# Optimization experiments

Hardware: AMD Instinct MI355X
Metric: run time of the kernel (lower is better)

Reference implementation:

```python
import jax, jax.numpy as jnp
import numpy as np

N_USER = 100000
N_ITEM = 100000
E = 500000
EMB, HID, OUT = 128, 128, 64


def _mean_agg(msg_src, src, dst, n_dst):
    """Gather per-edge messages from src nodes, segment-mean onto dst nodes."""
    m = msg_src[src]  # [E, d]
    s = jax.ops.segment_sum(m, dst, num_segments=n_dst)
    cnt = jax.ops.segment_sum(jnp.ones((src.shape[0],), m.dtype), dst,
                              num_segments=n_dst)
    # DGL mean reducer yields 0 for nodes with no in-edges
    return jnp.where(cnt[:, None] > 0, s / jnp.maximum(cnt, 1.0)[:, None], 0.0)


def _layer(feat_u, feat_i, W0, b0, Wui, bui, Wiu, biu,
           src_ui, dst_ui, src_iu, dst_iu):
    # shared self-transform (weight0) -> residual h0 on every ntype
    h0_u = feat_u @ W0 + b0
    h0_i = feat_i @ W0 + b0
    # per-etype transform of source features
    wh_u = feat_u @ Wui + bui  # messages along user->item
    wh_i = feat_i @ Wiu + biu  # messages along item->user
    h_i = _mean_agg(wh_u, src_ui, dst_ui, N_ITEM) + h0_i
    h_u = _mean_agg(wh_i, src_iu, dst_iu, N_USER) + h0_u
    return h_u, h_i


def setup_inputs() -> dict:
    key = jax.random.key(0)
    ks = jax.random.split(key, 12)
    sc_e = 1.0 / np.sqrt(EMB)
    sc_h = 1.0 / np.sqrt(HID)
    return {
        "emb_user": jax.random.normal(ks[0], (N_USER, EMB), jnp.float32),
        "emb_item": jax.random.normal(ks[1], (N_ITEM, EMB), jnp.float32),
        "W1_0": jax.random.normal(ks[2], (EMB, HID), jnp.float32) * sc_e,
        "b1_0": jnp.zeros((HID,), jnp.float32),
        "W1_ui": jax.random.normal(ks[3], (EMB, HID), jnp.float32) * sc_e,
        "b1_ui": jnp.zeros((HID,), jnp.float32),
        "W1_iu": jax.random.normal(ks[4], (EMB, HID), jnp.float32) * sc_e,
        "b1_iu": jnp.zeros((HID,), jnp.float32),
        "W2_0": jax.random.normal(ks[5], (HID, OUT), jnp.float32) * sc_h,
        "b2_0": jnp.zeros((OUT,), jnp.float32),
        "W2_ui": jax.random.normal(ks[6], (HID, OUT), jnp.float32) * sc_h,
        "b2_ui": jnp.zeros((OUT,), jnp.float32),
        "W2_iu": jax.random.normal(ks[7], (HID, OUT), jnp.float32) * sc_h,
        "b2_iu": jnp.zeros((OUT,), jnp.float32),
        "src_ui": jax.random.randint(ks[8], (E,), 0, N_USER, jnp.int32),
        "dst_ui": jax.random.randint(ks[9], (E,), 0, N_ITEM, jnp.int32),
        "src_iu": jax.random.randint(ks[10], (E,), 0, N_ITEM, jnp.int32),
        "dst_iu": jax.random.randint(ks[11], (E,), 0, N_USER, jnp.int32),
    }


def reference(emb_user, emb_item,
              W1_0, b1_0, W1_ui, b1_ui, W1_iu, b1_iu,
              W2_0, b2_0, W2_ui, b2_ui, W2_iu, b2_iu,
              src_ui, dst_ui, src_iu, dst_iu):
    h_u, h_i = _layer(emb_user, emb_item, W1_0, b1_0, W1_ui, b1_ui,
                      W1_iu, b1_iu, src_ui, dst_ui, src_iu, dst_iu)
    h_u = jax.nn.leaky_relu(h_u, 0.01)  # torch F.leaky_relu default slope
    h_i = jax.nn.leaky_relu(h_i, 0.01)
    h_u, h_i = _layer(h_u, h_i, W2_0, b2_0, W2_ui, b2_ui,
                      W2_iu, b2_iu, src_ui, dst_ui, src_iu, dst_iu)
    return h_u, h_i
```

## Files before the change

kernel.cpp:

```cpp
#include <hip/hip_runtime.h>

#define N_USER 100000
#define N_ITEM 100000
#define NEDGE  500000
#define DEGCAP 32

#define B_FILL 256
#define B_CONV 12500
#define B_WT   384
#define B_TOT  (B_FILL + B_CONV + B_WT)

typedef __attribute__((ext_vector_type(8))) short short8;
typedef __attribute__((ext_vector_type(4))) float f32x4;

__device__ __forceinline__ unsigned short f2bf(float f) {
  union { float f; unsigned int u; } x{f};
  unsigned int r = x.u + 0x7fffu + ((x.u >> 16) & 1u);
  return (unsigned short)(r >> 16);
}
__device__ __forceinline__ float bf2f(unsigned short u) {
  union { unsigned int u; float f; } x{(unsigned int)u << 16};
  return x.f;
}

__global__ __launch_bounds__(256) void setup_k(
    const int* __restrict__ src_ui, const int* __restrict__ dst_ui,
    int* __restrict__ cur_i, int* __restrict__ csr_ui,
    const int* __restrict__ src_iu, const int* __restrict__ dst_iu,
    int* __restrict__ cur_u, int* __restrict__ csr_iu,
    const float* __restrict__ emb_u, const float* __restrict__ emb_i,
    unsigned short* __restrict__ ebu, unsigned short* __restrict__ ebi,
    const float* __restrict__ W10, const float* __restrict__ W1ui,
    const float* __restrict__ W1iu, const float* __restrict__ W20,
    const float* __restrict__ W2ui, const float* __restrict__ W2iu,
    unsigned short* __restrict__ WT1i, unsigned short* __restrict__ WT1u,
    unsigned short* __restrict__ WT2i, unsigned short* __restrict__ WT2u) {
  int b = blockIdx.x, tid = threadIdx.x;
  if (b < B_FILL) {
    int chunk = b * 4096;
#pragma unroll 1
    for (int it = 0; it < 4; ++it) {
      int e0 = chunk + it * 1024 + tid;
      int d[4], s[4];
      int* curp[4]; int* csrp[4];
      bool ok[4];
#pragma unroll
      for (int k = 0; k < 4; ++k) {
        int e = e0 + k * 256;
        ok[k] = (e < 2 * NEDGE);
        bool g0 = (e < NEDGE);
        int ee = g0 ? e : e - NEDGE;
        const int* dp = g0 ? dst_ui : dst_iu;
        const int* sp = g0 ? src_ui : src_iu;
        curp[k] = g0 ? cur_i : cur_u;
        csrp[k] = g0 ? csr_ui : csr_iu;
        d[k] = ok[k] ? dp[ee] : 0;
        s[k] = ok[k] ? sp[ee] : 0;
      }
      int p[4];
#pragma unroll
      for (int k = 0; k < 4; ++k)
        p[k] = ok[k] ? atomicAdd(&curp[k][d[k]], 1) : DEGCAP;
#pragma unroll
      for (int k = 0; k < 4; ++k)
        if (ok[k] && p[k] < DEGCAP) csrp[k][d[k] * DEGCAP + p[k]] = s[k];
    }
  } else if (b < B_FILL + B_CONV) {
    int blk = b - B_FILL;
    const float* src; unsigned short* dstp;
    if (blk < 6250) { src = emb_u; dstp = ebu; }
    else { blk -= 6250; src = emb_i; dstp = ebi; }
    size_t g = (size_t)blk * 2048 + (size_t)tid * 8;
    float4 x = *(const float4*)(src + g);
    float4 y = *(const float4*)(src + g + 4);
    short8 v{(short)f2bf(x.x), (short)f2bf(x.y), (short)f2bf(x.z), (short)f2bf(x.w),
             (short)f2bf(y.x), (short)f2bf(y.y), (short)f2bf(y.z), (short)f2bf(y.w)};
    *(short8*)(dstp + g) = v;
  } else {
    int t = (b - B_FILL - B_CONV) * 256 + tid;
    if (t < 32768) {
      int n = t >> 8, k = t & 255;
      float v = (k < 128) ? W10[k * 128 + n] : W1ui[(k - 128) * 128 + n];
      WT1i[t] = f2bf(v);
    } else if (t < 65536) {
      int q = t - 32768; int n = q >> 8, k = q & 255;
      float v = (k < 128) ? W10[k * 128 + n] : W1iu[(k - 128) * 128 + n];
      WT1u[q] = f2bf(v);
    } else if (t < 81920) {
      int q = t - 65536; int n = q >> 8, k = q & 255;
      float v = (k < 128) ? W20[k * 64 + n] : W2ui[(k - 128) * 64 + n];
      WT2i[q] = f2bf(v);
    } else {
      int q = t - 81920; int n = q >> 8, k = q & 255;
      float v = (k < 128) ? W20[k * 64 + n] : W2iu[(k - 128) * 64 + n];
      WT2u[q] = f2bf(v);
    }
  }
}

__global__ __launch_bounds__(256) void aggc_k(
    const unsigned short* __restrict__ featA, const int* __restrict__ curA,
    const int* __restrict__ csrA, unsigned short* __restrict__ outA,
    const unsigned short* __restrict__ featB, const int* __restrict__ curB,
    const int* __restrict__ csrB, unsigned short* __restrict__ outB,
    int nbA) {
  __shared__ int sidx[16][32];
  int b = blockIdx.x;
  const unsigned short* feat; const int* cur; const int* csr; unsigned short* out;
  if (b < nbA) { feat = featA; cur = curA; csr = csrA; out = outA; }
  else { b -= nbA; feat = featB; cur = curB; csr = csrB; out = outB; }
  int grp = threadIdx.x >> 4;
  int ln  = threadIdx.x & 15;
  int node = b * 16 + grp;
  int deg = min(cur[node], DEGCAP);

  int2 sl = *(const int2*)(csr + (size_t)node * DEGCAP + ln * 2);
  sidx[grp][ln * 2] = sl.x;
  sidx[grp][ln * 2 + 1] = sl.y;
  __syncthreads();

  const int* lidx = sidx[grp];
  float a[8] = {0, 0, 0, 0, 0, 0, 0, 0};
  int j = 0;
  if (j + 4 <= deg) {
    int i0 = lidx[0], i1 = lidx[1], i2 = lidx[2], i3 = lidx[3];
    for (;;) {
      bool more = (j + 8 <= deg);
      int n0, n1, n2, n3;
      if (more) { n0 = lidx[j + 4]; n1 = lidx[j + 5]; n2 = lidx[j + 6]; n3 = lidx[j + 7]; }
      short8 v0 = *(const short8*)(feat + (size_t)i0 * 128 + ln * 8);
      short8 v1 = *(const short8*)(feat + (size_t)i1 * 128 + ln * 8);
      short8 v2 = *(const short8*)(feat + (size_t)i2 * 128 + ln * 8);
      short8 v3 = *(const short8*)(feat + (size_t)i3 * 128 + ln * 8);
#pragma unroll
      for (int d = 0; d < 8; ++d)
        a[d] += (bf2f((unsigned short)v0[d]) + bf2f((unsigned short)v1[d])) +
                (bf2f((unsigned short)v2[d]) + bf2f((unsigned short)v3[d]));
      j += 4;
      if (!more) break;
      i0 = n0; i1 = n1; i2 = n2; i3 = n3;
    }
  }
  if (j + 2 <= deg) {
    int i0 = lidx[j], i1 = lidx[j + 1];
    short8 v0 = *(const short8*)(feat + (size_t)i0 * 128 + ln * 8);
    short8 v1 = *(const short8*)(feat + (size_t)i1 * 128 + ln * 8);
#pragma unroll
    for (int d = 0; d < 8; ++d)
      a[d] += bf2f((unsigned short)v0[d]) + bf2f((unsigned short)v1[d]);
    j += 2;
  }
  if (j < deg) {
    short8 v = *(const short8*)(feat + (size_t)lidx[j] * 128 + ln * 8);
#pragma unroll
    for (int d = 0; d < 8; ++d) a[d] += bf2f((unsigned short)v[d]);
  }
  float sc = deg ? 1.f / (float)deg : 0.f;
  short8 pk;
#pragma unroll
  for (int d = 0; d < 8; ++d) pk[d] = (short)f2bf(a[d] * sc);
  *(short8*)(out + (size_t)node * 128 + ln * 8) = pk;
}

template <int N, bool LRELU, bool OUTBF16>
__global__ __launch_bounds__(256) void gemm2_k(
    const unsigned short* __restrict__ A1a, const unsigned short* __restrict__ A2a,
    const unsigned short* __restrict__ WTa, const float* __restrict__ b0a,
    const float* __restrict__ bea, const int* __restrict__ cura,
    void* __restrict__ outa,
    const unsigned short* __restrict__ A1b, const unsigned short* __restrict__ A2b,
    const unsigned short* __restrict__ WTb, const float* __restrict__ b0b,
    const float* __restrict__ beb, const int* __restrict__ curb,
    void* __restrict__ outb, int M, int nbA) {
  constexpr int BM = 64;
  constexpr int CPW = N / 4;
  constexpr int NCF = CPW / 16;
  __shared__ short As[BM * 128];
  __shared__ short Ws[N * 128];
  __shared__ float degmask[BM];

  int blk = blockIdx.x;
  const unsigned short* A1; const unsigned short* A2; const unsigned short* WT;
  const float* b0; const float* be; const int* cur; void* outv;
  if (blk < nbA) { A1 = A1a; A2 = A2a; WT = WTa; b0 = b0a; be = bea; cur = cura; outv = outa; }
  else { blk -= nbA; A1 = A1b; A2 = A2b; WT = WTb; b0 = b0b; be = beb; cur = curb; outv = outb; }

  const int tid = threadIdx.x;
  const int lane = tid & 63;
  const int wave = tid >> 6;
  const int row0 = blk * BM;
  const int colbase = wave * CPW;

  short8 aA[4], aB[4];
#pragma unroll
  for (int it = 0; it < 4; ++it) {
    int chunk = tid + it * 256;
    int row = chunk >> 4, c16 = chunk & 15;
    int gr = row0 + row; if (gr > M - 1) gr = M - 1;
    aA[it] = *(const short8*)(A1 + (size_t)gr * 128 + c16 * 8);
    aB[it] = *(const short8*)(A2 + (size_t)gr * 128 + c16 * 8);
  }

  if (tid < BM) {
    int r = row0 + tid;
    degmask[tid] = (r < M && cur[r] > 0) ? 1.f : 0.f;
  }

  f32x4 acc[4][NCF] = {};

#pragma unroll
  for (int kh = 0; kh < 2; ++kh) {
    __syncthreads();
#pragma unroll
    for (int it = 0; it < 4; ++it) {
      int chunk = tid + it * 256;
      int row = chunk >> 4, c16 = chunk & 15;
      int byteoff = row * 256 + ((c16 * 16) ^ ((row & 7) << 4));
      *(short8*)((char*)As + byteoff) = (kh == 0) ? aA[it] : aB[it];
    }
#pragma unroll
    for (int it = 0; it < (N * 16) / 256; ++it) {
      int chunk = tid + it * 256;
      int n = chunk >> 4, c16 = chunk & 15;
      short8 v = *(const short8*)(WT + (size_t)n * 256 + kh * 128 + c16 * 8);
      int byteoff = n * 256 + ((c16 * 16) ^ ((n & 7) << 4));
      *(short8*)((char*)Ws + byteoff) = v;
    }
    __syncthreads();

#pragma unroll
    for (int ks = 0; ks < 4; ++ks) {
      short8 af[4];
#pragma unroll
      for (int rf = 0; rf < 4; ++rf) {
        int row = rf * 16 + (lane & 15);
        int c16 = ks * 4 + (lane >> 4);
        int byteoff = row * 256 + ((c16 * 16) ^ ((row & 7) << 4));
        af[rf] = *(const short8*)((const char*)As + byteoff);
      }
      short8 wf[NCF];
#pragma unroll
      for (int cf = 0; cf < NCF; ++cf) {
        int n = colbase + cf * 16 + (lane & 15);
        int c16 = ks * 4 + (lane >> 4);
        int byteoff = n * 256 + ((c16 * 16) ^ ((n & 7) << 4));
        wf[cf] = *(const short8*)((const char*)Ws + byteoff);
      }
#pragma unroll
      for (int rf = 0; rf < 4; ++rf)
#pragma unroll
        for (int cf = 0; cf < NCF; ++cf)
          acc[rf][cf] = __builtin_amdgcn_mfma_f32_16x16x32_bf16(
              af[rf], wf[cf], acc[rf][cf], 0, 0, 0);
    }
  }

#pragma unroll
  for (int cf = 0; cf < NCF; ++cf) {
    int c = colbase + cf * 16 + (lane & 15);
    float bb0 = b0[c], bbe = be[c];
#pragma unroll
    for (int rf = 0; rf < 4; ++rf) {
#pragma unroll
      for (int j = 0; j < 4; ++j) {
        int lr = rf * 16 + (lane >> 4) * 4 + j;
        int r = row0 + lr;
        if (r < M) {
          float v = acc[rf][cf][j] + bb0 + degmask[lr] * bbe;
          if (LRELU) v = (v >= 0.f) ? v : 0.01f * v;
          if (OUTBF16)
            ((unsigned short*)outv)[(size_t)r * N + c] = f2bf(v);
          else
            ((float*)outv)[(size_t)r * N + c] = v;
        }
      }
    }
  }
}

extern "C" void kernel_launch(void* const* d_in, const int* in_sizes, int n_in,
                              void* d_out, int out_size, void* d_ws,
                              size_t ws_size, hipStream_t stream) {
  const float* emb_u = (const float*)d_in[0];
  const float* emb_i = (const float*)d_in[1];
  const float* W1_0  = (const float*)d_in[2];
  const float* b1_0  = (const float*)d_in[3];
  const float* W1_ui = (const float*)d_in[4];
  const float* b1_ui = (const float*)d_in[5];
  const float* W1_iu = (const float*)d_in[6];
  const float* b1_iu = (const float*)d_in[7];
  const float* W2_0  = (const float*)d_in[8];
  const float* b2_0  = (const float*)d_in[9];
  const float* W2_ui = (const float*)d_in[10];
  const float* b2_ui = (const float*)d_in[11];
  const float* W2_iu = (const float*)d_in[12];
  const float* b2_iu = (const float*)d_in[13];
  const int* src_ui = (const int*)d_in[14];
  const int* dst_ui = (const int*)d_in[15];
  const int* src_iu = (const int*)d_in[16];
  const int* dst_iu = (const int*)d_in[17];
  float* out = (float*)d_out;

  char* p = (char*)d_ws;
  unsigned short* WT1i = (unsigned short*)p; p += 65536;
  unsigned short* WT1u = (unsigned short*)p; p += 65536;
  unsigned short* WT2i = (unsigned short*)p; p += 32768;
  unsigned short* WT2u = (unsigned short*)p; p += 32768;
  int* cur_i = (int*)p; p += 400128;
  int* cur_u = (int*)p; p += 400128;
  int* csr_ui = (int*)p; p += (size_t)100032 * DEGCAP * 4;
  int* csr_iu = (int*)p; p += (size_t)100032 * DEGCAP * 4;
  const size_t FB = (size_t)N_USER * 128 * 2;
  unsigned short* ebu  = (unsigned short*)p; p += FB;
  unsigned short* ebi  = (unsigned short*)p; p += FB;
  unsigned short* hu = ebu;
  unsigned short* hi = ebi;
  unsigned short* aggB = (unsigned short*)out;
  unsigned short* aggA = (unsigned short*)(out + (size_t)N_USER * 64);

  const int GG = (N_USER + 63) / 64;

  hipMemsetAsync(cur_i, 0, 2 * 400128, stream);
  setup_k<<<B_TOT, 256, 0, stream>>>(src_ui, dst_ui, cur_i, csr_ui,
                                     src_iu, dst_iu, cur_u, csr_iu,
                                     emb_u, emb_i, ebu, ebi,
                                     W1_0, W1_ui, W1_iu, W2_0, W2_ui, W2_iu,
                                     WT1i, WT1u, WT2i, WT2u);

  aggc_k<<<2 * 6250, 256, 0, stream>>>(
      ebu, cur_i, csr_ui, aggA, ebi, cur_u, csr_iu, aggB, 6250);
  gemm2_k<128, true, true><<<2 * GG, 256, 0, stream>>>(
      ebi, aggA, WT1i, b1_0, b1_ui, cur_i, hi,
      ebu, aggB, WT1u, b1_0, b1_iu, cur_u, hu, N_USER, GG);

  aggc_k<<<2 * 6250, 256, 0, stream>>>(
      hu, cur_i, csr_ui, aggA, hi, cur_u, csr_iu, aggB, 6250);
  gemm2_k<64, false, false><<<2 * GG, 256, 0, stream>>>(
      hi, aggA, WT2i, b2_0, b2_ui, cur_i, out + (size_t)N_USER * 64,
      hu, aggB, WT2u, b2_0, b2_iu, cur_u, out, N_USER, GG);
}
```

Measured before the change: 225.9 us.

## Transform layer-2 messages before aggregation to gather 64-wide rows instead of 128

Layer 2 previously aggregated the 128-wide hidden features and then multiplied by the edge weights. Mean aggregation commutes with the linear map, so the message transform (h @ W2_e) is now fused into the layer-1 GEMM epilogue, which writes 64-wide bf16 messages. A new 64-wide gather kernel averages those, and a simplified layer-2 GEMM applies only the self weight plus the aggregated term. This halves the gather traffic for layer 2 and shrinks its GEMM. The cost is extra workspace, an extra MFMA stage and LDS round-trip in gemm1, and one more bf16 rounding of the messages before averaging.

```diff
diff --git a/kernel.cpp b/kernel.cpp
--- a/kernel.cpp
+++ b/kernel.cpp
@@ -11,6 +11,7 @@
 #define B_TOT  (B_FILL + B_CONV + B_WT)
 
 typedef __attribute__((ext_vector_type(8))) short short8;
+typedef __attribute__((ext_vector_type(4))) short short4_t;
 typedef __attribute__((ext_vector_type(4))) float f32x4;
 
 __device__ __forceinline__ unsigned short f2bf(float f) {
@@ -162,34 +163,95 @@
   *(short8*)(out + (size_t)node * 128 + ln * 8) = pk;
 }
 
-template <int N, bool LRELU, bool OUTBF16>
-__global__ __launch_bounds__(256) void gemm2_k(
+__global__ __launch_bounds__(256) void agg64_k(
+    const unsigned short* __restrict__ featA, const int* __restrict__ curA,
+    const int* __restrict__ csrA, unsigned short* __restrict__ outA,
+    const unsigned short* __restrict__ featB, const int* __restrict__ curB,
+    const int* __restrict__ csrB, unsigned short* __restrict__ outB,
+    int nbA) {
+  __shared__ int sidx[16][32];
+  int b = blockIdx.x;
+  const unsigned short* feat; const int* cur; const int* csr; unsigned short* out;
+  if (b < nbA) { feat = featA; cur = curA; csr = csrA; out = outA; }
+  else { b -= nbA; feat = featB; cur = curB; csr = csrB; out = outB; }
+  int grp = threadIdx.x >> 4;
+  int ln  = threadIdx.x & 15;
+  int node = b * 16 + grp;
+  int deg = min(cur[node], DEGCAP);
+
+  int2 sl = *(const int2*)(csr + (size_t)node * DEGCAP + ln * 2);
+  sidx[grp][ln * 2] = sl.x;
+  sidx[grp][ln * 2 + 1] = sl.y;
+  __syncthreads();
+
+  const int* lidx = sidx[grp];
+  float a[4] = {0, 0, 0, 0};
+  int j = 0;
+  if (j + 4 <= deg) {
+    int i0 = lidx[0], i1 = lidx[1], i2 = lidx[2], i3 = lidx[3];
+    for (;;) {
+      bool more = (j + 8 <= deg);
+      int n0, n1, n2, n3;
+      if (more) { n0 = lidx[j + 4]; n1 = lidx[j + 5]; n2 = lidx[j + 6]; n3 = lidx[j + 7]; }
+      short4_t v0 = *(const short4_t*)(feat + (size_t)i0 * 64 + ln * 4);
+      short4_t v1 = *(const short4_t*)(feat + (size_t)i1 * 64 + ln * 4);
+      short4_t v2 = *(const short4_t*)(feat + (size_t)i2 * 64 + ln * 4);
+      short4_t v3 = *(const short4_t*)(feat + (size_t)i3 * 64 + ln * 4);
+#pragma unroll
+      for (int d = 0; d < 4; ++d)
+        a[d] += (bf2f((unsigned short)v0[d]) + bf2f((unsigned short)v1[d])) +
+                (bf2f((unsigned short)v2[d]) + bf2f((unsigned short)v3[d]));
+      j += 4;
+      if (!more) break;
+      i0 = n0; i1 = n1; i2 = n2; i3 = n3;
+    }
+  }
+  if (j + 2 <= deg) {
+    int i0 = lidx[j], i1 = lidx[j + 1];
+    short4_t v0 = *(const short4_t*)(feat + (size_t)i0 * 64 + ln * 4);
+    short4_t v1 = *(const short4_t*)(feat + (size_t)i1 * 64 + ln * 4);
+#pragma unroll
+    for (int d = 0; d < 4; ++d)
+      a[d] += bf2f((unsigned short)v0[d]) + bf2f((unsigned short)v1[d]);
+    j += 2;
+  }
+  if (j < deg) {
+    short4_t v = *(const short4_t*)(feat + (size_t)lidx[j] * 64 + ln * 4);
+#pragma unroll
+    for (int d = 0; d < 4; ++d) a[d] += bf2f((unsigned short)v[d]);
+  }
+  float sc = deg ? 1.f / (float)deg : 0.f;
+  short4_t pk;
+#pragma unroll
+  for (int d = 0; d < 4; ++d) pk[d] = (short)f2bf(a[d] * sc);
+  *(short4_t*)(out + (size_t)node * 64 + ln * 4) = pk;
+}
+
+__global__ __launch_bounds__(256) void gemm1_k(
     const unsigned short* __restrict__ A1a, const unsigned short* __restrict__ A2a,
-    const unsigned short* __restrict__ WTa, const float* __restrict__ b0a,
+    const unsigned short* __restrict__ WT1a, const float* __restrict__ b0a,
     const float* __restrict__ bea, const int* __restrict__ cura,
-    void* __restrict__ outa,
+    unsigned short* __restrict__ outa, const unsigned short* __restrict__ WT2ea,
+    unsigned short* __restrict__ wh2a,
     const unsigned short* __restrict__ A1b, const unsigned short* __restrict__ A2b,
-    const unsigned short* __restrict__ WTb, const float* __restrict__ b0b,
+    const unsigned short* __restrict__ WT1b, const float* __restrict__ b0b,
     const float* __restrict__ beb, const int* __restrict__ curb,
-    void* __restrict__ outb, int M, int nbA) {
-  constexpr int BM = 64;
-  constexpr int CPW = N / 4;
-  constexpr int NCF = CPW / 16;
-  __shared__ short As[BM * 128];
-  __shared__ short Ws[N * 128];
-  __shared__ float degmask[BM];
+    unsigned short* __restrict__ outb, const unsigned short* __restrict__ WT2eb,
+    unsigned short* __restrict__ wh2b, int M, int nbA) {
+  __shared__ short As[64 * 128];
+  __shared__ short Ws[128 * 128];
+  __shared__ float degmask[64];
 
   int blk = blockIdx.x;
-  const unsigned short* A1; const unsigned short* A2; const unsigned short* WT;
-  const float* b0; const float* be; const int* cur; void* outv;
-  if (blk < nbA) { A1 = A1a; A2 = A2a; WT = WTa; b0 = b0a; be = bea; cur = cura; outv = outa; }
-  else { blk -= nbA; A1 = A1b; A2 = A2b; WT = WTb; b0 = b0b; be = beb; cur = curb; outv = outb; }
+  const unsigned short *A1, *A2, *WT1, *WT2e; const float *b0, *be;
+  const int* cur; unsigned short *outp, *wh2;
+  if (blk < nbA) { A1 = A1a; A2 = A2a; WT1 = WT1a; b0 = b0a; be = bea; cur = cura; outp = outa; WT2e = WT2ea; wh2 = wh2a; }
+  else { blk -= nbA; A1 = A1b; A2 = A2b; WT1 = WT1b; b0 = b0b; be = beb; cur = curb; outp = outb; WT2e = WT2eb; wh2 = wh2b; }
 
   const int tid = threadIdx.x;
   const int lane = tid & 63;
   const int wave = tid >> 6;
-  const int row0 = blk * BM;
-  const int colbase = wave * CPW;
+  const int row0 = blk * 64;
 
   short8 aA[4], aB[4];
 #pragma unroll
@@ -201,12 +263,12 @@
     aB[it] = *(const short8*)(A2 + (size_t)gr * 128 + c16 * 8);
   }
 
-  if (tid < BM) {
+  if (tid < 64) {
     int r = row0 + tid;
     degmask[tid] = (r < M && cur[r] > 0) ? 1.f : 0.f;
   }
 
-  f32x4 acc[4][NCF] = {};
+  f32x4 acc[4][2] = {};
 
 #pragma unroll
   for (int kh = 0; kh < 2; ++kh) {
@@ -219,10 +281,10 @@
       *(short8*)((char*)As + byteoff) = (kh == 0) ? aA[it] : aB[it];
     }
 #pragma unroll
-    for (int it = 0; it < (N * 16) / 256; ++it) {
+    for (int it = 0; it < 8; ++it) {
       int chunk = tid + it * 256;
       int n = chunk >> 4, c16 = chunk & 15;
-      short8 v = *(const short8*)(WT + (size_t)n * 256 + kh * 128 + c16 * 8);
+      short8 v = *(const short8*)(WT1 + (size_t)n * 256 + kh * 128 + c16 * 8);
       int byteoff = n * 256 + ((c16 * 16) ^ ((n & 7) << 4));
       *(short8*)((char*)Ws + byteoff) = v;
     }
@@ -238,10 +300,10 @@
         int byteoff = row * 256 + ((c16 * 16) ^ ((row & 7) << 4));
         af[rf] = *(const short8*)((const char*)As + byteoff);
       }
-      short8 wf[NCF];
-#pragma unroll
-      for (int cf = 0; cf < NCF; ++cf) {
-        int n = colbase + cf * 16 + (lane & 15);
+      short8 wf[2];
+#pragma unroll
+      for (int cf = 0; cf < 2; ++cf) {
+        int n = wave * 32 + cf * 16 + (lane & 15);
         int c16 = ks * 4 + (lane >> 4);
         int byteoff = n * 256 + ((c16 * 16) ^ ((n & 7) << 4));
         wf[cf] = *(const short8*)((const char*)Ws + byteoff);
@@ -249,32 +311,168 @@
 #pragma unroll
       for (int rf = 0; rf < 4; ++rf)
 #pragma unroll
-        for (int cf = 0; cf < NCF; ++cf)
+        for (int cf = 0; cf < 2; ++cf)
           acc[rf][cf] = __builtin_amdgcn_mfma_f32_16x16x32_bf16(
               af[rf], wf[cf], acc[rf][cf], 0, 0, 0);
     }
   }
 
-#pragma unroll
-  for (int cf = 0; cf < NCF; ++cf) {
-    int c = colbase + cf * 16 + (lane & 15);
+  __syncthreads();
+
+#pragma unroll
+  for (int cf = 0; cf < 2; ++cf) {
+    int c = wave * 32 + cf * 16 + (lane & 15);
     float bb0 = b0[c], bbe = be[c];
 #pragma unroll
     for (int rf = 0; rf < 4; ++rf) {
+#pragma unroll
+      for (int j = 0; j < 4; ++j) {
+        int lr = rf * 16 + (lane >> 4) * 4 + j;
+        int r = row0 + lr;
+        float v = acc[rf][cf][j] + bb0 + degmask[lr] * bbe;
+        v = (v >= 0.f) ? v : 0.01f * v;
+        unsigned short hb = f2bf(v);
+        if (r < M) outp[(size_t)r * 128 + c] = hb;
+        int byteoff = lr * 256 + (((c >> 3) << 4) ^ ((lr & 7) << 4)) + ((c * 2) & 15);
+        *(short*)((char*)As + byteoff) = (short)hb;
+      }
+    }
+  }
+#pragma unroll
+  for (int it = 0; it < 4; ++it) {
+    int chunk = tid + it * 256;
+    int n = chunk >> 4, c16 = chunk & 15;
+    short8 v = *(const short8*)(WT2e + (size_t)n * 256 + 128 + c16 * 8);
+    int byteoff = n * 256 + ((c16 * 16) ^ ((n & 7) << 4));
+    *(short8*)((char*)Ws + byteoff) = v;
+  }
+  __syncthreads();
+
+  f32x4 acc2[4] = {};
+#pragma unroll
+  for (int ks = 0; ks < 4; ++ks) {
+    short8 af[4];
+#pragma unroll
+    for (int rf = 0; rf < 4; ++rf) {
+      int row = rf * 16 + (lane & 15);
+      int c16 = ks * 4 + (lane >> 4);
+      int byteoff = row * 256 + ((c16 * 16) ^ ((row & 7) << 4));
+      af[rf] = *(const short8*)((const char*)As + byteoff);
+    }
+    short8 wf;
+    {
+      int n = wave * 16 + (lane & 15);
+      int c16 = ks * 4 + (lane >> 4);
+      int byteoff = n * 256 + ((c16 * 16) ^ ((n & 7) << 4));
+      wf = *(const short8*)((const char*)Ws + byteoff);
+    }
+#pragma unroll
+    for (int rf = 0; rf < 4; ++rf)
+      acc2[rf] = __builtin_amdgcn_mfma_f32_16x16x32_bf16(af[rf], wf, acc2[rf], 0, 0, 0);
+  }
+  {
+    int c = wave * 16 + (lane & 15);
+#pragma unroll
+    for (int rf = 0; rf < 4; ++rf)
+#pragma unroll
+      for (int j = 0; j < 4; ++j) {
+        int r = row0 + rf * 16 + (lane >> 4) * 4 + j;
+        if (r < M) wh2[(size_t)r * 64 + c] = f2bf(acc2[rf][j]);
+      }
+  }
+}
+
+__global__ __launch_bounds__(256) void gemm2s_k(
+    const unsigned short* __restrict__ A1a, const unsigned short* __restrict__ agga,
+    const unsigned short* __restrict__ WTa, const float* __restrict__ b0a,
+    const float* __restrict__ bea, const int* __restrict__ cura,
+    float* __restrict__ outa,
+    const unsigned short* __restrict__ A1b, const unsigned short* __restrict__ aggb,
+    const unsigned short* __restrict__ WTb, const float* __restrict__ b0b,
+    const float* __restrict__ beb, const int* __restrict__ curb,
+    float* __restrict__ outb, int M, int nbA) {
+  __shared__ short As[64 * 128];
+  __shared__ short Ws[64 * 128];
+  __shared__ float degmask[64];
+
+  int blk = blockIdx.x;
+  const unsigned short *A1, *agg, *WT; const float *b0, *be; const int* cur;
+  float* outp;
+  if (blk < nbA) { A1 = A1a; agg = agga; WT = WTa; b0 = b0a; be = bea; cur = cura; outp = outa; }
+  else { blk -= nbA; A1 = A1b; agg = aggb; WT = WTb; b0 = b0b; be = beb; cur = curb; outp = outb; }
+
+  const int tid = threadIdx.x;
+  const int lane = tid & 63;
+  const int wave = tid >> 6;
+  const int row0 = blk * 64;
+
+  short8 aA[4];
+#pragma unroll
+  for (int it = 0; it < 4; ++it) {
+    int chunk = tid + it * 256;
+    int row = chunk >> 4, c16 = chunk & 15;
+    int gr = row0 + row; if (gr > M - 1) gr = M - 1;
+    aA[it] = *(const short8*)(A1 + (size_t)gr * 128 + c16 * 8);
+  }
+  if (tid < 64) {
+    int r = row0 + tid;
+    degmask[tid] = (r < M && cur[r] > 0) ? 1.f : 0.f;
+  }
+#pragma unroll
+  for (int it = 0; it < 4; ++it) {
+    int chunk = tid + it * 256;
+    int row = chunk >> 4, c16 = chunk & 15;
+    int byteoff = row * 256 + ((c16 * 16) ^ ((row & 7) << 4));
+    *(short8*)((char*)As + byteoff) = aA[it];
+  }
+#pragma unroll
+  for (int it = 0; it < 4; ++it) {
+    int chunk = tid + it * 256;
+    int n = chunk >> 4, c16 = chunk & 15;
+    short8 v = *(const short8*)(WT + (size_t)n * 256 + c16 * 8);
+    int byteoff = n * 256 + ((c16 * 16) ^ ((n & 7) << 4));
+    *(short8*)((char*)Ws + byteoff) = v;
+  }
+  __syncthreads();
+
+  f32x4 acc[4] = {};
+#pragma unroll
+  for (int ks = 0; ks < 4; ++ks) {
+    short8 af[4];
+#pragma unroll
+    for (int rf = 0; rf < 4; ++rf) {
+      int row = rf * 16 + (lane & 15);
+      int c16 = ks * 4 + (lane >> 4);
+      int byteoff = row * 256 + ((c16 * 16) ^ ((row & 7) << 4));
+      af[rf] = *(const short8*)((const char*)As + byteoff);
+    }
+    short8 wf;
+    {
+      int n = wave * 16 + (lane & 15);
+      int c16 = ks * 4 + (lane >> 4);
+      int byteoff = n * 256 + ((c16 * 16) ^ ((n & 7) << 4));
+      wf = *(const short8*)((const char*)Ws + byteoff);
+    }
+#pragma unroll
+    for (int rf = 0; rf < 4; ++rf)
+      acc[rf] = __builtin_amdgcn_mfma_f32_16x16x32_bf16(af[rf], wf, acc[rf], 0, 0, 0);
+  }
+
+  {
+    int c = wave * 16 + (lane & 15);
+    float bb0 = b0[c], bbe = be[c];
+#pragma unroll
+    for (int rf = 0; rf < 4; ++rf)
 #pragma unroll
       for (int j = 0; j < 4; ++j) {
         int lr = rf * 16 + (lane >> 4) * 4 + j;
         int r = row0 + lr;
         if (r < M) {
-          float v = acc[rf][cf][j] + bb0 + degmask[lr] * bbe;
-          if (LRELU) v = (v >= 0.f) ? v : 0.01f * v;
-          if (OUTBF16)
-            ((unsigned short*)outv)[(size_t)r * N + c] = f2bf(v);
-          else
-            ((float*)outv)[(size_t)r * N + c] = v;
+          float v = acc[rf][j] + bf2f(agg[(size_t)r * 64 + c]) + bb0 +
+                    degmask[lr] * bbe;
+          outp[(size_t)r * 64 + c] = v;
         }
       }
-    }
   }
 }
 
@@ -313,6 +511,11 @@
   const size_t FB = (size_t)N_USER * 128 * 2;
   unsigned short* ebu  = (unsigned short*)p; p += FB;
   unsigned short* ebi  = (unsigned short*)p; p += FB;
+  const size_t HB = (size_t)100032 * 64 * 2;
+  unsigned short* wh2u = (unsigned short*)p; p += HB;
+  unsigned short* wh2i = (unsigned short*)p; p += HB;
+  unsigned short* ag64A = (unsigned short*)p; p += HB;
+  unsigned short* ag64B = (unsigned short*)p; p += HB;
   unsigned short* hu = ebu;
   unsigned short* hi = ebi;
   unsigned short* aggB = (unsigned short*)out;
@@ -329,13 +532,14 @@
 
   aggc_k<<<2 * 6250, 256, 0, stream>>>(
       ebu, cur_i, csr_ui, aggA, ebi, cur_u, csr_iu, aggB, 6250);
-  gemm2_k<128, true, true><<<2 * GG, 256, 0, stream>>>(
-      ebi, aggA, WT1i, b1_0, b1_ui, cur_i, hi,
-      ebu, aggB, WT1u, b1_0, b1_iu, cur_u, hu, N_USER, GG);
-
-  aggc_k<<<2 * 6250, 256, 0, stream>>>(
-      hu, cur_i, csr_ui, aggA, hi, cur_u, csr_iu, aggB, 6250);
-  gemm2_k<64, false, false><<<2 * GG, 256, 0, stream>>>(
-      hi, aggA, WT2i, b2_0, b2_ui, cur_i, out + (size_t)N_USER * 64,
-      hu, aggB, WT2u, b2_0, b2_iu, cur_u, out, N_USER, GG);
-}
+  gemm1_k<<<2 * GG, 256, 0, stream>>>(
+      ebi, aggA, WT1i, b1_0, b1_ui, cur_i, hi, WT2u, wh2i,
+      ebu, aggB, WT1u, b1_0, b1_iu, cur_u, hu, WT2i, wh2u,
+      N_USER, GG);
+
+  agg64_k<<<2 * 6250, 256, 0, stream>>>(
+      wh2u, cur_i, csr_ui, ag64A, wh2i, cur_u, csr_iu, ag64B, 6250);
+  gemm2s_k<<<2 * GG, 256, 0, stream>>>(
+      hi, ag64A, WT2i, b2_0, b2_ui, cur_i, out + (size_t)N_USER * 64,
+      hu, ag64B, WT2u, b2_0, b2_iu, cur_u, out, N_USER, GG);
+}
```

New measurement: 225.8 us, median of 2. No clear change (-0.0%).
